# Performance work log

Hardware: AMD Instinct MI355X
Metric: run time of the kernel (lower is better)

## Reference

```python
import jax, jax.numpy as jnp
import numpy as np
import math

NH = 71      # Falcon-7B query heads (MQA: 1 shared K head, 1 shared V head)
HD = 64      # head dim
H = NH * HD  # 4544
S = 2048
ROPE_BASE = 10000.0


def _rope_tables(seq_len, dim, dtype):
    inv_freq = 1.0 / (ROPE_BASE ** (jnp.arange(0, dim, 2, dtype=jnp.float32) / dim))
    t = jnp.arange(seq_len, dtype=jnp.float32)
    freqs = jnp.outer(t, inv_freq)              # [S, dim/2]
    emb = jnp.concatenate([freqs, freqs], -1)   # [S, dim]
    return jnp.cos(emb).astype(dtype), jnp.sin(emb).astype(dtype)


def _rotate_half(x):
    x1, x2 = x[..., : HD // 2], x[..., HD // 2 :]
    return jnp.concatenate([-x2, x1], axis=-1)


def _apply_rope(x, cos, sin):
    # x: [..., S, HD]; cos/sin: [S, HD]
    return x * cos + _rotate_half(x) * sin


def setup_inputs() -> dict:
    key = jax.random.key(0)
    k0, k1, k2 = jax.random.split(key, 3)
    hidden_states = jax.random.normal(k0, (1, 1, S, H), dtype=jnp.float32)
    qkv_w = jax.random.normal(k1, (H, (NH + 2) * HD), dtype=jnp.float32) * 0.02
    dense_w = jax.random.normal(k2, (H, H), dtype=jnp.float32) * 0.02
    # additive causal mask (0 on/below diagonal, large negative above)
    causal = jnp.tril(jnp.ones((S, S), dtype=bool))
    attention_mask = jnp.where(causal, 0.0, -1e9).astype(jnp.float32)[None, None]
    return {"hidden_states": hidden_states, "attention_mask": attention_mask,
            "qkv_w": qkv_w, "dense_w": dense_w}


def reference(hidden_states, attention_mask, qkv_w, dense_w):
    x = hidden_states[0, 0]                       # [S, H]
    qkv = x @ qkv_w                               # [S, (NH+2)*HD]
    q = qkv[:, : NH * HD].reshape(S, NH, HD).transpose(1, 0, 2)  # [NH, S, HD]
    k = qkv[:, NH * HD : (NH + 1) * HD]           # [S, HD] shared K head
    v = qkv[:, (NH + 1) * HD :]                   # [S, HD] shared V head

    cos, sin = _rope_tables(S, HD, x.dtype)
    q = _apply_rope(q, cos[None], sin[None])
    k = _apply_rope(k, cos, sin)

    scale = 1.0 / math.sqrt(HD)
    scores = jnp.einsum("hsd,td->hst", q, k) * scale + attention_mask[0, 0]
    probs = jax.nn.softmax(scores, axis=-1)       # [NH, S, S]
    attn = jnp.einsum("hst,td->hsd", probs, v)    # [NH, S, HD]

    attn = attn.transpose(1, 0, 2).reshape(S, H)  # concat heads
    out = attn @ dense_w                          # [S, H]
    return out[None, None]                        # [1, 1, S, H]
```

## Files before the change

kernel.cpp:

```cpp
#include <hip/hip_runtime.h>
#include <hip/hip_bf16.h>
#include <math.h>

#define S_LEN 2048
#define NHEADS 71
#define HDIM 64
#define HSZ (NHEADS * HDIM)
#define QKVN ((NHEADS + 2) * HDIM)
#define QKVP 4736
#define DNP  4608

typedef unsigned short u16;
typedef __attribute__((ext_vector_type(8))) short short8;
typedef __attribute__((ext_vector_type(4))) short bfx4;
typedef __attribute__((ext_vector_type(4))) float floatx4;

__device__ __forceinline__ float bf2f(u16 v) {
    unsigned u = ((unsigned)v) << 16;
    return __builtin_bit_cast(float, u);
}
__device__ __forceinline__ u16 f2bf(float f) {
    unsigned u = __builtin_bit_cast(unsigned, f);
    u += 0x7fff + ((u >> 16) & 1);
    return (u16)(u >> 16);
}

__device__ __forceinline__ void async16(const u16* g, u16* l) {
    __builtin_amdgcn_global_load_lds(
        (const __attribute__((address_space(1))) void*)g,
        (__attribute__((address_space(3))) void*)l,
        16, 0, 0);
}

__global__ __launch_bounds__(256) void convert_bf16(const float* __restrict__ src,
                                                    u16* __restrict__ dst, int n)
{
    int i = (blockIdx.x * 256 + threadIdx.x) * 8;
    if (i >= n) return;
    floatx4 a = *(const floatx4*)(src + i);
    floatx4 b = *(const floatx4*)(src + i + 4);
    u16 o[8];
#pragma unroll
    for (int j = 0; j < 4; ++j) { o[j] = f2bf(a[j]); o[4 + j] = f2bf(b[j]); }
    *(short8*)(dst + i) = *(short8*)&o[0];
}

__global__ __launch_bounds__(256) void conv_transpose(const float* __restrict__ src,
                                                      u16* __restrict__ dst,
                                                      int K, int Ns)
{
    __shared__ float t[32][33];
    const int k0 = blockIdx.x * 32, n0 = blockIdx.y * 32;
    const int tx = threadIdx.x & 31, ty = threadIdx.x >> 5;
#pragma unroll
    for (int i = 0; i < 4; ++i) {
        int r = ty + i * 8;
        int n = n0 + tx;
        t[r][tx] = (n < Ns) ? src[(size_t)(k0 + r) * Ns + n] : 0.f;
    }
    __syncthreads();
#pragma unroll
    for (int i = 0; i < 4; ++i) {
        int rr = ty + i * 8;
        dst[(size_t)(n0 + rr) * K + k0 + tx] = f2bf(t[tx][rr]);
    }
}

template <bool STORE_F32>
__global__ __launch_bounds__(256) void gemm128(const u16* __restrict__ A,
                                               const u16* __restrict__ Bt,
                                               void* __restrict__ Cv,
                                               int M, int K, int Np, int Nreal)
{
    __shared__ u16 As[2 * 128 * 64];
    __shared__ u16 Bs[2 * 128 * 64];

    const int tid  = threadIdx.x;
    const int w    = tid >> 6, lane = tid & 63;
    const int l15  = lane & 15, quad = lane >> 4;

    int bx = blockIdx.x, by = blockIdx.y;
    {
        const int nbx = gridDim.x, nby = gridDim.y;
        const int nwg = nbx * nby;
        if ((nwg & 7) == 0) {
            const int L   = by * nbx + bx;
            const int g   = L & 7;
            const int s   = L >> 3;
            const int CM  = g * (nwg >> 3) + s;
            bx = CM / nby;
            by = CM % nby;
        }
    }
    const int bm = by * 128, bn = bx * 128;
    const int wm = (w >> 1) * 64, wn = (w & 1) * 64;

    floatx4 acc[4][4] = {};

    const int srow = w * 32 + (lane >> 3);
    const int scol = (((lane & 7) ^ ((lane >> 3) & 7)) * 8);
    const u16* Ab = A  + (size_t)(bm + srow) * K + scol;
    const u16* Bb = Bt + (size_t)(bn + srow) * K + scol;
    const int woff = (w * 32) * 64;

    const int nkt = K >> 6;

#pragma unroll
    for (int i = 0; i < 4; ++i)
        async16(Ab + (size_t)(i * 8) * K, As + woff + i * 8 * 64);
#pragma unroll
    for (int i = 0; i < 4; ++i)
        async16(Bb + (size_t)(i * 8) * K, Bs + woff + i * 8 * 64);
    __syncthreads();

    for (int t = 0; t < nkt; ++t) {
        const int cur = t & 1;
        const u16* Asc = As + cur * (128 * 64);
        const u16* Bsc = Bs + cur * (128 * 64);

        if (t + 1 < nkt) {
            const int kb = (t + 1) << 6;
            u16* Asn = As + (cur ^ 1) * (128 * 64) + woff;
            u16* Bsn = Bs + (cur ^ 1) * (128 * 64) + woff;
#pragma unroll
            for (int i = 0; i < 4; ++i)
                async16(Ab + (size_t)(i * 8) * K + kb, Asn + i * 8 * 64);
#pragma unroll
            for (int i = 0; i < 4; ++i)
                async16(Bb + (size_t)(i * 8) * K + kb, Bsn + i * 8 * 64);
        }

        const int rk = l15 & 7;
#pragma unroll
        for (int kk = 0; kk < 2; ++kk) {
            short8 af[4], bfr[4];
#pragma unroll
            for (int tt = 0; tt < 4; ++tt) {
                const int slotA = ((kk * 4 + quad) ^ rk) * 8;
                af[tt]  = *(const short8*)&Asc[(wm + tt * 16 + l15) * 64 + slotA];
                bfr[tt] = *(const short8*)&Bsc[(wn + tt * 16 + l15) * 64 + slotA];
            }
#pragma unroll
            for (int mi = 0; mi < 4; ++mi)
#pragma unroll
                for (int ni = 0; ni < 4; ++ni)
                    acc[mi][ni] = __builtin_amdgcn_mfma_f32_16x16x32_bf16(
                        af[mi], bfr[ni], acc[mi][ni], 0, 0, 0);
        }

        __syncthreads();
    }

    if (STORE_F32) {
        float* C = (float*)Cv;
#pragma unroll
        for (int mi = 0; mi < 4; ++mi)
#pragma unroll
            for (int ni = 0; ni < 4; ++ni) {
                int col  = bn + wn + ni * 16 + l15;
                int row0 = bm + wm + mi * 16 + quad * 4;
                if (col < Nreal) {
#pragma unroll
                    for (int r = 0; r < 4; ++r)
                        C[(size_t)(row0 + r) * Nreal + col] = acc[mi][ni][r];
                }
            }
    } else {
        u16* C = (u16*)Cv;
#pragma unroll
        for (int mi = 0; mi < 4; ++mi)
#pragma unroll
            for (int ni = 0; ni < 4; ++ni) {
                int col  = bn + wn + ni * 16 + l15;
                int row0 = bm + wm + mi * 16 + quad * 4;
#pragma unroll
                for (int r = 0; r < 4; ++r)
                    C[(size_t)(row0 + r) * Np + col] = f2bf(acc[mi][ni][r]);
            }
    }
}

__global__ void rope_kv(const u16* __restrict__ qkv, int QP,
                        u16* __restrict__ Kr,
                        u16* __restrict__ VT)
{
    int idx = blockIdx.x * 256 + threadIdx.x;
    int s = idx >> 7;
    int c = idx & 127;
    if (c < HDIM) {
        int d = c;
        float x  = bf2f(qkv[(size_t)s * QP + HSZ + d]);
        int dp   = (d < 32) ? d + 32 : d - 32;
        float rot = (d < 32) ? -bf2f(qkv[(size_t)s * QP + HSZ + dp])
                             :  bf2f(qkv[(size_t)s * QP + HSZ + dp]);
        float invf = expf(-(float)(d & 31) * 0.28782313662425572f);
        float ang  = (float)s * invf;
        float o = x * cosf(ang) + rot * sinf(ang);
        Kr[(size_t)s * HDIM + d] = f2bf(o);
    } else {
        int d = c - HDIM;
        VT[(size_t)d * S_LEN + s] = qkv[(size_t)s * QP + (NHEADS + 1) * HDIM + d];
    }
}

__global__ __launch_bounds__(256) void attn2(const u16* __restrict__ qkv, int QP,
                                             const u16* __restrict__ Kr,
                                             const u16* __restrict__ VT,
                                             u16* __restrict__ O)
{
    __shared__ u16 Kt[128][72];
    __shared__ u16 Vt[64][136];

    const int tid  = threadIdx.x;
    const int h    = blockIdx.x;
    const int qt   = 31 - blockIdx.y;
    const int qs   = qt * 64;
    const int w    = tid >> 6;
    const int lane = tid & 63;
    const int l15  = lane & 15;
    const int quad = lane >> 4;

    const int q_row = qs + w * 16 + l15;
    const u16* qp = qkv + (size_t)q_row * QP + h * HDIM;
    short8 r0 = *(const short8*)(qp + quad * 8);
    short8 r1 = *(const short8*)(qp + 32 + quad * 8);
    short8 qf0, qf1;
#pragma unroll
    for (int j = 0; j < 8; ++j) {
        int d0 = quad * 8 + j;
        float invf = expf(-(float)d0 * 0.28782313662425572f);
        float ang  = (float)q_row * invf;
        float cs = cosf(ang), sn = sinf(ang);
        float x0 = bf2f((u16)r0[j]), x1 = bf2f((u16)r1[j]);
        qf0[j] = (short)f2bf((x0 * cs - x1 * sn) * 0.125f);
        qf1[j] = (short)f2bf((x1 * cs + x0 * sn) * 0.125f);
    }

    floatx4 ot0 = {0.f,0.f,0.f,0.f}, ot1 = {0.f,0.f,0.f,0.f};
    floatx4 ot2 = {0.f,0.f,0.f,0.f}, ot3 = {0.f,0.f,0.f,0.f};
    float m_p = -1e30f, l_p = 0.f;
    const int qmin_w  = qs + w * 16;
    const int nchunks = (qt + 2) >> 1;

    const int krow = tid >> 1, kcol = (tid & 1) * 32;
    const int vrow = tid >> 2, vcol = (tid & 3) * 32;

    for (int c = 0; c < nchunks; ++c) {
        const int cbase = c * 128;

        const u16* kp = Kr + (size_t)(cbase + krow) * HDIM + kcol;
        short8 k0 = *(const short8*)(kp);
        short8 k1 = *(const short8*)(kp + 8);
        short8 k2 = *(const short8*)(kp + 16);
        short8 k3 = *(const short8*)(kp + 24);
        const u16* vp = VT + (size_t)vrow * S_LEN + cbase + vcol;
        short8 v0 = *(const short8*)(vp);
        short8 v1 = *(const short8*)(vp + 8);
        short8 v2 = *(const short8*)(vp + 16);
        short8 v3 = *(const short8*)(vp + 24);
        __syncthreads();
        *(short8*)&Kt[krow][kcol]      = k0;
        *(short8*)&Kt[krow][kcol + 8]  = k1;
        *(short8*)&Kt[krow][kcol + 16] = k2;
        *(short8*)&Kt[krow][kcol + 24] = k3;
        *(short8*)&Vt[vrow][vcol]      = v0;
        *(short8*)&Vt[vrow][vcol + 8]  = v1;
        *(short8*)&Vt[vrow][vcol + 16] = v2;
        *(short8*)&Vt[vrow][vcol + 24] = v3;
        __syncthreads();

        const int nsub = min(8, ((qmin_w - cbase) >> 4) + 1);

        floatx4 sc[8];
        float tmax = -3e38f;
#pragma unroll
        for (int s = 0; s < 8; ++s) {
            if (s < nsub) {
                short8 ka = *(const short8*)&Kt[s * 16 + l15][quad * 8];
                short8 kb = *(const short8*)&Kt[s * 16 + l15][32 + quad * 8];
                floatx4 a = {0.f,0.f,0.f,0.f};
                __builtin_amdgcn_s_setprio(1);
                a = __builtin_amdgcn_mfma_f32_16x16x32_bf16(ka, qf0, a, 0, 0, 0);
                a = __builtin_amdgcn_mfma_f32_16x16x32_bf16(kb, qf1, a, 0, 0, 0);
                __builtin_amdgcn_s_setprio(0);
                if (cbase + s * 16 + 15 > qmin_w) {
                    int tb = cbase + s * 16 + quad * 4;
#pragma unroll
                    for (int r = 0; r < 4; ++r)
                        if (tb + r > q_row) a[r] = -1e30f;
                }
                sc[s] = a;
                tmax = fmaxf(tmax, fmaxf(fmaxf(a[0], a[1]), fmaxf(a[2], a[3])));
            }
        }
        tmax = fmaxf(tmax, __shfl_xor(tmax, 16, 64));
        tmax = fmaxf(tmax, __shfl_xor(tmax, 32, 64));

        float mnew = fmaxf(m_p, tmax);
        float al   = __expf(m_p - mnew);
        m_p = mnew;
        ot0 *= al; ot1 *= al; ot2 *= al; ot3 *= al;

        float lsum = 0.f;
#pragma unroll
        for (int s = 0; s < 8; s += 2) {
            if (s < nsub) {
                const bool two = (s + 1 < nsub);
                float p0 = __expf(sc[s][0] - mnew);
                float p1 = __expf(sc[s][1] - mnew);
                float p2 = __expf(sc[s][2] - mnew);
                float p3 = __expf(sc[s][3] - mnew);
                float p4 = 0.f, p5 = 0.f, p6 = 0.f, p7 = 0.f;
                if (two) {
                    p4 = __expf(sc[s + 1][0] - mnew);
                    p5 = __expf(sc[s + 1][1] - mnew);
                    p6 = __expf(sc[s + 1][2] - mnew);
                    p7 = __expf(sc[s + 1][3] - mnew);
                }
                lsum += ((p0 + p1) + (p2 + p3)) + ((p4 + p5) + (p6 + p7));
                short8 pb = { (short)f2bf(p0), (short)f2bf(p1),
                              (short)f2bf(p2), (short)f2bf(p3),
                              (short)f2bf(p4), (short)f2bf(p5),
                              (short)f2bf(p6), (short)f2bf(p7) };
                const int vc0 = s * 16 + quad * 4;
                const int vc1 = vc0 + 16;
                bfx4 z = {0, 0, 0, 0};
                bfx4 lo0 = *(const bfx4*)&Vt[l15][vc0];
                bfx4 lo1 = *(const bfx4*)&Vt[16 + l15][vc0];
                bfx4 lo2 = *(const bfx4*)&Vt[32 + l15][vc0];
                bfx4 lo3 = *(const bfx4*)&Vt[48 + l15][vc0];
                bfx4 hi0 = z, hi1 = z, hi2 = z, hi3 = z;
                if (two) {
                    hi0 = *(const bfx4*)&Vt[l15][vc1];
                    hi1 = *(const bfx4*)&Vt[16 + l15][vc1];
                    hi2 = *(const bfx4*)&Vt[32 + l15][vc1];
                    hi3 = *(const bfx4*)&Vt[48 + l15][vc1];
                }
                short8 a0 = { lo0[0], lo0[1], lo0[2], lo0[3], hi0[0], hi0[1], hi0[2], hi0[3] };
                short8 a1 = { lo1[0], lo1[1], lo1[2], lo1[3], hi1[0], hi1[1], hi1[2], hi1[3] };
                short8 a2 = { lo2[0], lo2[1], lo2[2], lo2[3], hi2[0], hi2[1], hi2[2], hi2[3] };
                short8 a3 = { lo3[0], lo3[1], lo3[2], lo3[3], hi3[0], hi3[1], hi3[2], hi3[3] };
                __builtin_amdgcn_s_setprio(1);
                ot0 = __builtin_amdgcn_mfma_f32_16x16x32_bf16(a0, pb, ot0, 0, 0, 0);
                ot1 = __builtin_amdgcn_mfma_f32_16x16x32_bf16(a1, pb, ot1, 0, 0, 0);
                ot2 = __builtin_amdgcn_mfma_f32_16x16x32_bf16(a2, pb, ot2, 0, 0, 0);
                ot3 = __builtin_amdgcn_mfma_f32_16x16x32_bf16(a3, pb, ot3, 0, 0, 0);
                __builtin_amdgcn_s_setprio(0);
            }
        }
        lsum += __shfl_xor(lsum, 16, 64);
        lsum += __shfl_xor(lsum, 32, 64);
        l_p = l_p * al + lsum;
    }

    float inv = 1.0f / l_p;
    u16* op = O + (size_t)q_row * HSZ + h * HDIM + quad * 4;
    bfx4 s0 = { (short)f2bf(ot0[0]*inv), (short)f2bf(ot0[1]*inv),
                (short)f2bf(ot0[2]*inv), (short)f2bf(ot0[3]*inv) };
    bfx4 s1 = { (short)f2bf(ot1[0]*inv), (short)f2bf(ot1[1]*inv),
                (short)f2bf(ot1[2]*inv), (short)f2bf(ot1[3]*inv) };
    bfx4 s2 = { (short)f2bf(ot2[0]*inv), (short)f2bf(ot2[1]*inv),
                (short)f2bf(ot2[2]*inv), (short)f2bf(ot2[3]*inv) };
    bfx4 s3 = { (short)f2bf(ot3[0]*inv), (short)f2bf(ot3[1]*inv),
                (short)f2bf(ot3[2]*inv), (short)f2bf(ot3[3]*inv) };
    *(bfx4*)(op)      = s0;
    *(bfx4*)(op + 16) = s1;
    *(bfx4*)(op + 32) = s2;
    *(bfx4*)(op + 48) = s3;
}

extern "C" void kernel_launch(void* const* d_in, const int* in_sizes, int n_in,
                              void* d_out, int out_size, void* d_ws, size_t ws_size,
                              hipStream_t stream)
{
    const float* x       = (const float*)d_in[0];
    const float* qkv_w   = (const float*)d_in[2];
    const float* dense_w = (const float*)d_in[3];
    for (int i = 0; i < n_in; ++i) {
        if (in_sizes[i] == S_LEN * HSZ)      x       = (const float*)d_in[i];
        else if (in_sizes[i] == HSZ * QKVN)  qkv_w   = (const float*)d_in[i];
        else if (in_sizes[i] == HSZ * HSZ)   dense_w = (const float*)d_in[i];
    }
    float* out = (float*)d_out;

    const size_t E_XB  = (size_t)S_LEN * HSZ;
    const size_t E_WT  = (size_t)QKVP * HSZ;
    const size_t E_QKV = (size_t)S_LEN * QKVP;
    const size_t E_KV  = (size_t)S_LEN * HDIM;

    u16* xb_at = (u16*)d_ws;
    u16* wt    = xb_at + E_XB;
    u16* qkvp  = wt + E_WT;
    u16* kr    = qkvp + E_QKV;
    u16* vt    = kr + E_KV;

    convert_bf16<<<(int)(E_XB / 8 / 256), 256, 0, stream>>>(x, xb_at, (int)E_XB);
    conv_transpose<<<dim3(HSZ / 32, QKVP / 32), 256, 0, stream>>>(qkv_w, wt, HSZ, QKVN);
    gemm128<false><<<dim3(QKVP / 128, S_LEN / 128), 256, 0, stream>>>(
        xb_at, wt, qkvp, S_LEN, HSZ, QKVP, QKVN);
    conv_transpose<<<dim3(HSZ / 32, DNP / 32), 256, 0, stream>>>(dense_w, wt, HSZ, HSZ);
    rope_kv<<<(S_LEN * 2 * HDIM) / 256, 256, 0, stream>>>(qkvp, QKVP, kr, vt);
    attn2<<<dim3(NHEADS, 32), 256, 0, stream>>>(qkvp, QKVP, kr, vt, xb_at);
    gemm128<true><<<dim3(DNP / 128, S_LEN / 128), 256, 0, stream>>>(
        xb_at, wt, out, S_LEN, HSZ, DNP, HSZ);
}
```

Measured before the change: 654.4 us.

## Load GEMM A fragments directly from global into registers, drop A shared tile

The gemm128 kernel no longer stages the A tile through LDS. Each wave loads its A MFMA fragments straight from global memory into registers and prefetches the next K-step while computing the current one. This removes the A LDS writes and reads and halves shared memory use, which may allow higher occupancy. In exchange, A rows are shared by the two waves with the same wm, so each is fetched from global twice, the register footprint grows, and the per-lane global loads are strided rather than coalesced.

```diff
diff --git a/kernel.cpp b/kernel.cpp
--- a/kernel.cpp
+++ b/kernel.cpp
@@ -72,7 +72,6 @@
                                                void* __restrict__ Cv,
                                                int M, int K, int Np, int Nreal)
 {
-    __shared__ u16 As[2 * 128 * 64];
     __shared__ u16 Bs[2 * 128 * 64];
 
     const int tid  = threadIdx.x;
@@ -99,56 +98,64 @@
 
     const int srow = w * 32 + (lane >> 3);
     const int scol = (((lane & 7) ^ ((lane >> 3) & 7)) * 8);
-    const u16* Ab = A  + (size_t)(bm + srow) * K + scol;
-    const u16* Bb = Bt + (size_t)(bn + srow) * K + scol;
+    const u16* Bb  = Bt + (size_t)(bn + srow) * K + scol;
     const int woff = (w * 32) * 64;
 
+    const u16* Ar[4];
+#pragma unroll
+    for (int mi = 0; mi < 4; ++mi)
+        Ar[mi] = A + (size_t)(bm + wm + mi * 16 + l15) * K + quad * 8;
+
     const int nkt = K >> 6;
 
-#pragma unroll
-    for (int i = 0; i < 4; ++i)
-        async16(Ab + (size_t)(i * 8) * K, As + woff + i * 8 * 64);
 #pragma unroll
     for (int i = 0; i < 4; ++i)
         async16(Bb + (size_t)(i * 8) * K, Bs + woff + i * 8 * 64);
+    short8 afc[8], afn[8];
+#pragma unroll
+    for (int kk = 0; kk < 2; ++kk)
+#pragma unroll
+        for (int mi = 0; mi < 4; ++mi)
+            afc[kk * 4 + mi] = *(const short8*)(Ar[mi] + kk * 32);
     __syncthreads();
 
     for (int t = 0; t < nkt; ++t) {
         const int cur = t & 1;
-        const u16* Asc = As + cur * (128 * 64);
         const u16* Bsc = Bs + cur * (128 * 64);
+        const int kbn = (t + 1 < nkt) ? ((t + 1) << 6) : 0;
 
         if (t + 1 < nkt) {
-            const int kb = (t + 1) << 6;
-            u16* Asn = As + (cur ^ 1) * (128 * 64) + woff;
             u16* Bsn = Bs + (cur ^ 1) * (128 * 64) + woff;
 #pragma unroll
             for (int i = 0; i < 4; ++i)
-                async16(Ab + (size_t)(i * 8) * K + kb, Asn + i * 8 * 64);
-#pragma unroll
-            for (int i = 0; i < 4; ++i)
-                async16(Bb + (size_t)(i * 8) * K + kb, Bsn + i * 8 * 64);
+                async16(Bb + (size_t)(i * 8) * K + kbn, Bsn + i * 8 * 64);
         }
+#pragma unroll
+        for (int kk = 0; kk < 2; ++kk)
+#pragma unroll
+            for (int mi = 0; mi < 4; ++mi)
+                afn[kk * 4 + mi] = *(const short8*)(Ar[mi] + kbn + kk * 32);
 
         const int rk = l15 & 7;
 #pragma unroll
         for (int kk = 0; kk < 2; ++kk) {
-            short8 af[4], bfr[4];
+            short8 bfr[4];
 #pragma unroll
             for (int tt = 0; tt < 4; ++tt) {
-                const int slotA = ((kk * 4 + quad) ^ rk) * 8;
-                af[tt]  = *(const short8*)&Asc[(wm + tt * 16 + l15) * 64 + slotA];
-                bfr[tt] = *(const short8*)&Bsc[(wn + tt * 16 + l15) * 64 + slotA];
+                const int slotB = ((kk * 4 + quad) ^ rk) * 8;
+                bfr[tt] = *(const short8*)&Bsc[(wn + tt * 16 + l15) * 64 + slotB];
             }
 #pragma unroll
             for (int mi = 0; mi < 4; ++mi)
 #pragma unroll
                 for (int ni = 0; ni < 4; ++ni)
                     acc[mi][ni] = __builtin_amdgcn_mfma_f32_16x16x32_bf16(
-                        af[mi], bfr[ni], acc[mi][ni], 0, 0, 0);
+                        afc[kk * 4 + mi], bfr[ni], acc[mi][ni], 0, 0, 0);
         }
 
         __syncthreads();
+#pragma unroll
+        for (int i = 0; i < 8; ++i) afc[i] = afn[i];
     }
 
     if (STORE_F32) {
```

Result: slower. 812.1 us (+24.1%).
